# Performance work log

Measured on AMD Instinct MI355X. Metric: run time of the kernel, lower is better.

Reference implementation:

```python
import jax, jax.numpy as jnp
import numpy as np

D_IN = 768
D_SAE = 24576
BATCH = 2048
K = 64


def setup_inputs() -> dict:
    key = jax.random.key(0)
    k1, k2 = jax.random.split(key)
    x = jax.random.normal(k1, (BATCH, D_IN), dtype=jnp.float32)
    # kaiming-uniform-ish init then unit-norm rows (set_decoder_norm_to_unit_norm)
    bound = np.sqrt(6.0 / D_SAE)
    W_dec = jax.random.uniform(k2, (D_SAE, D_IN), minval=-bound, maxval=bound, dtype=jnp.float32)
    W_dec = W_dec / jnp.linalg.norm(W_dec, axis=1, keepdims=True)
    W_enc = W_dec.T  # tied at init (W_dec.t().clone())
    b_enc = jnp.zeros((D_SAE,), dtype=jnp.float32)
    b_dec = jnp.zeros((D_IN,), dtype=jnp.float32)
    return {"x": x, "W_enc": W_enc, "W_dec": W_dec, "b_enc": b_enc, "b_dec": b_dec, "k": K}


def topk_activation(pre, k):
    # torch.topk -> relu(values) -> scatter into zeros
    vals, idx = jax.lax.top_k(pre, k)            # [B, k]
    vals = jax.nn.relu(vals)
    rows = jnp.arange(pre.shape[0])[:, None]     # [B, 1]
    return jnp.zeros_like(pre).at[rows, idx].set(vals)


def reference(x, W_enc, W_dec, b_enc, b_dec, k):
    # normalize=False -> preprocess is identity
    xc = x - b_dec
    latents_pre_act = xc @ W_enc + b_enc         # [B, d_sae]
    latents = topk_activation(latents_pre_act, k)
    recons = latents @ W_dec + b_dec             # [B, d_in]
    mse_loss = jnp.sum((recons - x) ** 2)        # F.mse_loss(reduction='sum')
    return mse_loss
```

## Files before the change

### kernel.cpp

```cpp
#include <hip/hip_runtime.h>
#include <hip/hip_bf16.h>
#include <stdint.h>
#include <string.h>

#define D_IN 768
#define D_SAE 24576
#define BATCH 2048
#define TOPK 64

typedef _Float16 f16x8 __attribute__((ext_vector_type(8)));
typedef _Float16 f16x4 __attribute__((ext_vector_type(4)));
typedef float floatx4 __attribute__((ext_vector_type(4)));

#define AS1 __attribute__((address_space(1)))
#define AS3 __attribute__((address_space(3)))

__device__ __forceinline__ void load_lds16(const void* g, void* l) {
    __builtin_amdgcn_global_load_lds((AS1 void*)(g), (AS3 void*)(l), 16, 0, 0);
}

__global__ __launch_bounds__(256) void prep_x_kernel(const float* __restrict__ x,
                                                     const float* __restrict__ b_dec,
                                                     _Float16* __restrict__ xch,
                                                     float* __restrict__ out) {
    if (blockIdx.x == 0 && threadIdx.x == 0) out[0] = 0.0f;
    int i = (blockIdx.x * 256 + threadIdx.x) * 4;
    if (i >= BATCH * D_IN) return;
    int c = i % D_IN;
    float4 xv = *(const float4*)(x + i);
    float4 bv = *(const float4*)(b_dec + c);
    f16x4 h;
    h[0] = (_Float16)(xv.x - bv.x);
    h[1] = (_Float16)(xv.y - bv.y);
    h[2] = (_Float16)(xv.z - bv.z);
    h[3] = (_Float16)(xv.w - bv.w);
    *(f16x4*)(xch + i) = h;
}

__global__ __launch_bounds__(256) void transpose_kernel(const float* __restrict__ W,
                                                        _Float16* __restrict__ WT) {
    __shared__ _Float16 tile[32][33];
    int n0 = blockIdx.x * 32;
    int k0 = blockIdx.y * 32;
    int tx = threadIdx.x & 31, ty = threadIdx.x >> 5;
#pragma unroll
    for (int r = 0; r < 4; ++r) {
        int k = k0 + ty + r * 8;
        tile[ty + r * 8][tx] = (_Float16)W[(size_t)k * D_SAE + n0 + tx];
    }
    __syncthreads();
#pragma unroll
    for (int r = 0; r < 4; ++r) {
        int n = n0 + ty + r * 8;
        WT[(size_t)n * D_IN + k0 + tx] = tile[tx][ty + r * 8];
    }
}

__global__ __launch_bounds__(256) void gemm_kernel(const _Float16* __restrict__ A,
                                                   const _Float16* __restrict__ BT,
                                                   const float* __restrict__ b_enc,
                                                   unsigned short* __restrict__ pre) {
    __shared__ _Float16 As[128 * 32];
    __shared__ _Float16 Bs[128 * 32];
    const int tid = threadIdx.x;
    const int lane = tid & 63;
    const int wave = tid >> 6;
    const int m0 = blockIdx.x * 128;
    const int n0 = blockIdx.y * 128;
    const int wm = wave >> 1, wn = wave & 1;
    const int colv = lane & 15, quad = lane >> 4;

    floatx4 acc[4][4];
#pragma unroll
    for (int mi = 0; mi < 4; ++mi)
#pragma unroll
        for (int ni = 0; ni < 4; ++ni)
#pragma unroll
            for (int r = 0; r < 4; ++r) acc[mi][ni][r] = 0.0f;

    for (int kt = 0; kt < 24; ++kt) {
        const int k0 = kt * 32;
#pragma unroll
        for (int i = 0; i < 2; ++i) {
            int gw = i * 256 + wave * 64;
            int g = gw + lane;
            int r = g >> 2, kq = g & 3;
            load_lds16(A + (size_t)(m0 + r) * D_IN + k0 + kq * 8, &As[gw * 8]);
            load_lds16(BT + (size_t)(n0 + r) * D_IN + k0 + kq * 8, &Bs[gw * 8]);
        }
        __syncthreads();
        f16x8 af[4], bf[4];
#pragma unroll
        for (int mi = 0; mi < 4; ++mi)
            af[mi] = *(const f16x8*)&As[(wm * 64 + mi * 16 + colv) * 32 + quad * 8];
#pragma unroll
        for (int ni = 0; ni < 4; ++ni)
            bf[ni] = *(const f16x8*)&Bs[(wn * 64 + ni * 16 + colv) * 32 + quad * 8];
#pragma unroll
        for (int mi = 0; mi < 4; ++mi)
#pragma unroll
            for (int ni = 0; ni < 4; ++ni)
                acc[mi][ni] = __builtin_amdgcn_mfma_f32_16x16x32_f16(af[mi], bf[ni], acc[mi][ni], 0, 0, 0);
        __syncthreads();
    }
    float be[4];
#pragma unroll
    for (int ni = 0; ni < 4; ++ni) be[ni] = b_enc[n0 + wn * 64 + ni * 16 + colv];
#pragma unroll
    for (int mi = 0; mi < 4; ++mi) {
#pragma unroll
        for (int ni = 0; ni < 4; ++ni) {
            size_t base = (size_t)(m0 + wm * 64 + mi * 16 + quad * 4) * D_SAE
                        + (size_t)(n0 + wn * 64 + ni * 16 + colv);
#pragma unroll
            for (int r = 0; r < 4; ++r) {
                _Float16 h = (_Float16)(acc[mi][ni][r] + be[ni]);
                unsigned short u;
                __builtin_memcpy(&u, &h, 2);
                unsigned short key = u ^ ((u & 0x8000) ? 0xFFFFu : 0x8000u);
                pre[base + (size_t)r * D_SAE] = key;
            }
        }
    }
}

#define TKT 384
#define KPT 64
__global__ __launch_bounds__(TKT) void topk_loss_kernel(const unsigned short* __restrict__ pre,
                                                        const float* __restrict__ x,
                                                        const float* __restrict__ W_dec,
                                                        const float* __restrict__ b_dec,
                                                        float* __restrict__ out) {
    const int row = blockIdx.x;
    const int tid = threadIdx.x;
    const int lane = tid & 63, wv = tid >> 6;

    __shared__ int hist[256];
    __shared__ int wtot[6];
    __shared__ float wred[6];
    __shared__ int sh_cnt, sh_B, sh_K, na, ne;
    __shared__ int sel_idx[TOPK];
    __shared__ float sel_val[TOPK];

    const uint4* kp = (const uint4*)(pre + (size_t)row * D_SAE) + tid * 8;
    unsigned w[32];
#pragma unroll
    for (int i = 0; i < 8; ++i) {
        uint4 v = kp[i];
        w[i * 4 + 0] = v.x; w[i * 4 + 1] = v.y; w[i * 4 + 2] = v.z; w[i * 4 + 3] = v.w;
    }
    const int colbase = tid * KPT;

    if (tid == 0) sh_cnt = 0;
    __syncthreads();
    int c = 0;
#pragma unroll
    for (int q = 0; q < 32; ++q) {
        c += ((w[q] & 0xFFFFu) >= 0xC000u);
        c += ((w[q] >> 16) >= 0xC000u);
    }
#pragma unroll
    for (int off = 32; off > 0; off >>= 1) c += __shfl_down(c, off, 64);
    if (lane == 0) atomicAdd(&sh_cnt, c);
    __syncthreads();
    const unsigned lim = (sh_cnt >= TOPK) ? 0xC000u : 0u;

    if (tid < 256) hist[tid] = 0;
    __syncthreads();
#pragma unroll
    for (int q = 0; q < 32; ++q) {
        unsigned k0 = w[q] & 0xFFFFu, k1 = w[q] >> 16;
        if (k0 >= lim) atomicAdd(&hist[k0 >> 8], 1);
        if (k1 >= lim) atomicAdd(&hist[k1 >> 8], 1);
    }
    __syncthreads();
    int K = TOPK;
    {
        int h = 0, s = 0;
        if (tid < 256) { h = hist[tid]; s = h; }
#pragma unroll
        for (int off = 1; off < 64; off <<= 1) {
            int v = __shfl_down(s, off, 64);
            if (lane + off < 64) s += v;
        }
        if (tid < 256 && lane == 0) wtot[wv] = s;
        __syncthreads();
        if (tid < 256) {
            for (int w2 = wv + 1; w2 < 4; ++w2) s += wtot[w2];
            int G = s - h;
            if (G < K && s >= K) { sh_B = tid; sh_K = K - G; }
        }
        __syncthreads();
    }
    const unsigned B = (unsigned)sh_B;
    K = sh_K;
    __syncthreads();

    if (tid < 256) hist[tid] = 0;
    __syncthreads();
#pragma unroll
    for (int q = 0; q < 32; ++q) {
        unsigned k0 = w[q] & 0xFFFFu, k1 = w[q] >> 16;
        if ((k0 >> 8) == B) atomicAdd(&hist[k0 & 0xFF], 1);
        if ((k1 >> 8) == B) atomicAdd(&hist[k1 & 0xFF], 1);
    }
    __syncthreads();
    {
        int h = 0, s = 0;
        if (tid < 256) { h = hist[tid]; s = h; }
#pragma unroll
        for (int off = 1; off < 64; off <<= 1) {
            int v = __shfl_down(s, off, 64);
            if (lane + off < 64) s += v;
        }
        if (tid < 256 && lane == 0) wtot[wv] = s;
        __syncthreads();
        if (tid < 256) {
            for (int w2 = wv + 1; w2 < 4; ++w2) s += wtot[w2];
            int G = s - h;
            if (G < K && s >= K) { sh_B = tid; sh_K = K - G; }
        }
        __syncthreads();
    }
    const unsigned T = (B << 8) | (unsigned)sh_B;
    const int K2 = sh_K;
    const int nGreater = TOPK - K2;

    if (tid == 0) { na = 0; ne = 0; }
    __syncthreads();
#pragma unroll
    for (int q = 0; q < 32; ++q) {
#pragma unroll
        for (int half = 0; half < 2; ++half) {
            unsigned k = half ? (w[q] >> 16) : (w[q] & 0xFFFFu);
            int col = colbase + q * 2 + half;
            int slot = -1;
            if (k > T) slot = atomicAdd(&na, 1);
            else if (k == T) {
                int e = atomicAdd(&ne, 1);
                if (e < K2) slot = nGreater + e;
            }
            if (slot >= 0) {
                unsigned short u = (unsigned short)((k & 0x8000u) ? (k ^ 0x8000u) : (k ^ 0xFFFFu));
                _Float16 h;
                __builtin_memcpy(&h, &u, 2);
                float v = (float)h;
                sel_idx[slot] = col;
                sel_val[slot] = fmaxf(v, 0.0f);
            }
        }
    }
    __syncthreads();

    const int c0 = tid, c1 = tid + TKT;
    const float* xr = x + (size_t)row * D_IN;
    float r0 = b_dec[c0], r1 = b_dec[c1];
#pragma unroll 8
    for (int s = 0; s < TOPK; ++s) {
        float v = sel_val[s];
        const float* wr = W_dec + (size_t)sel_idx[s] * D_IN;
        r0 += v * wr[c0];
        r1 += v * wr[c1];
    }
    float d0 = r0 - xr[c0], d1 = r1 - xr[c1];
    float local = d0 * d0 + d1 * d1;

#pragma unroll
    for (int off = 32; off > 0; off >>= 1) local += __shfl_down(local, off, 64);
    if (lane == 0) wred[wv] = local;
    __syncthreads();
    if (tid == 0) {
        float s = 0.0f;
#pragma unroll
        for (int i = 0; i < 6; ++i) s += wred[i];
        atomicAdd(out, s);
    }
}

extern "C" void kernel_launch(void* const* d_in, const int* in_sizes, int n_in,
                              void* d_out, int out_size, void* d_ws, size_t ws_size,
                              hipStream_t stream) {
    const float* x     = (const float*)d_in[0];
    const float* W_enc = (const float*)d_in[1];
    const float* W_dec = (const float*)d_in[2];
    const float* b_enc = (const float*)d_in[3];
    const float* b_dec = (const float*)d_in[4];
    float* out = (float*)d_out;

    char* ws = (char*)d_ws;
    _Float16* xch      = (_Float16*)ws;
    _Float16* WT       = (_Float16*)(ws + 3145728);
    unsigned short* pre = (unsigned short*)(ws + 3145728 + 37748736);

    prep_x_kernel<<<1536, 256, 0, stream>>>(x, b_dec, xch, out);
    transpose_kernel<<<dim3(D_SAE / 32, D_IN / 32), 256, 0, stream>>>(W_enc, WT);
    gemm_kernel<<<dim3(BATCH / 128, D_SAE / 128), 256, 0, stream>>>(xch, WT, b_enc, pre);
    topk_loss_kernel<<<BATCH, TKT, 0, stream>>>(pre, x, W_dec, b_dec, out);
}
```

Measured before the change: 362.2 us.

## Collect top-k candidates above threshold in GEMM epilogue, select from compact list

The GEMM epilogue now appends every pre-activation whose key is at least fp16 2.0 to a per-row candidate list (key plus column), using a global atomic counter per row. The top-k kernel then runs its radix select over the small candidate list in LDS instead of rescanning the full 24576-wide row. It falls back to the full row if the count is below k or above capacity. This trades many global atomics in the GEMM epilogue for a large cut in top-k read traffic and work. The block size also drops to 256 threads.

```diff
diff --git a/kernel.cpp b/kernel.cpp
--- a/kernel.cpp
+++ b/kernel.cpp
@@ -7,6 +7,8 @@
 #define D_SAE 24576
 #define BATCH 2048
 #define TOPK 64
+#define CAP 1024
+#define KEY_LIM 0xC000u
 
 typedef _Float16 f16x8 __attribute__((ext_vector_type(8)));
 typedef _Float16 f16x4 __attribute__((ext_vector_type(4)));
@@ -22,9 +24,12 @@
 __global__ __launch_bounds__(256) void prep_x_kernel(const float* __restrict__ x,
                                                      const float* __restrict__ b_dec,
                                                      _Float16* __restrict__ xch,
+                                                     int* __restrict__ cnt,
                                                      float* __restrict__ out) {
-    if (blockIdx.x == 0 && threadIdx.x == 0) out[0] = 0.0f;
-    int i = (blockIdx.x * 256 + threadIdx.x) * 4;
+    int t = blockIdx.x * 256 + threadIdx.x;
+    if (t == 0) out[0] = 0.0f;
+    if (t < BATCH) cnt[t] = 0;
+    int i = t * 4;
     if (i >= BATCH * D_IN) return;
     int c = i % D_IN;
     float4 xv = *(const float4*)(x + i);
@@ -59,7 +64,9 @@
 __global__ __launch_bounds__(256) void gemm_kernel(const _Float16* __restrict__ A,
                                                    const _Float16* __restrict__ BT,
                                                    const float* __restrict__ b_enc,
-                                                   unsigned short* __restrict__ pre) {
+                                                   unsigned short* __restrict__ pre,
+                                                   int* __restrict__ cnt,
+                                                   unsigned* __restrict__ cand) {
     __shared__ _Float16 As[128 * 32];
     __shared__ _Float16 Bs[128 * 32];
     const int tid = threadIdx.x;
@@ -110,23 +117,29 @@
     for (int mi = 0; mi < 4; ++mi) {
 #pragma unroll
         for (int ni = 0; ni < 4; ++ni) {
-            size_t base = (size_t)(m0 + wm * 64 + mi * 16 + quad * 4) * D_SAE
-                        + (size_t)(n0 + wn * 64 + ni * 16 + colv);
+            const int n_g = n0 + wn * 64 + ni * 16 + colv;
+            const int r_g0 = m0 + wm * 64 + mi * 16 + quad * 4;
+            size_t base = (size_t)r_g0 * D_SAE + (size_t)n_g;
 #pragma unroll
             for (int r = 0; r < 4; ++r) {
                 _Float16 h = (_Float16)(acc[mi][ni][r] + be[ni]);
                 unsigned short u;
                 __builtin_memcpy(&u, &h, 2);
-                unsigned short key = u ^ ((u & 0x8000) ? 0xFFFFu : 0x8000u);
-                pre[base + (size_t)r * D_SAE] = key;
+                unsigned key = (unsigned)(u ^ ((u & 0x8000) ? 0xFFFFu : 0x8000u));
+                pre[base + (size_t)r * D_SAE] = (unsigned short)key;
+                if (key >= KEY_LIM) {
+                    int row = r_g0 + r;
+                    int slot = atomicAdd(&cnt[row], 1);
+                    if (slot < CAP) cand[(size_t)row * CAP + slot] = (key << 16) | (unsigned)n_g;
+                }
             }
         }
     }
 }
 
-#define TKT 384
-#define KPT 64
-__global__ __launch_bounds__(TKT) void topk_loss_kernel(const unsigned short* __restrict__ pre,
+__global__ __launch_bounds__(256) void topk_loss_kernel(const unsigned short* __restrict__ pre,
+                                                        const unsigned* __restrict__ cand,
+                                                        const int* __restrict__ cnt,
                                                         const float* __restrict__ x,
                                                         const float* __restrict__ W_dec,
                                                         const float* __restrict__ b_dec,
@@ -135,146 +148,120 @@
     const int tid = threadIdx.x;
     const int lane = tid & 63, wv = tid >> 6;
 
+    __shared__ unsigned cl[CAP];
     __shared__ int hist[256];
-    __shared__ int wtot[6];
-    __shared__ float wred[6];
-    __shared__ int sh_cnt, sh_B, sh_K, na, ne;
+    __shared__ int wtot[4];
+    __shared__ float wred[4];
+    __shared__ int sh_B, sh_K, na, ne;
     __shared__ int sel_idx[TOPK];
     __shared__ float sel_val[TOPK];
 
-    const uint4* kp = (const uint4*)(pre + (size_t)row * D_SAE) + tid * 8;
-    unsigned w[32];
-#pragma unroll
-    for (int i = 0; i < 8; ++i) {
-        uint4 v = kp[i];
-        w[i * 4 + 0] = v.x; w[i * 4 + 1] = v.y; w[i * 4 + 2] = v.z; w[i * 4 + 3] = v.w;
-    }
-    const int colbase = tid * KPT;
-
-    if (tid == 0) sh_cnt = 0;
-    __syncthreads();
-    int c = 0;
-#pragma unroll
-    for (int q = 0; q < 32; ++q) {
-        c += ((w[q] & 0xFFFFu) >= 0xC000u);
-        c += ((w[q] >> 16) >= 0xC000u);
-    }
-#pragma unroll
-    for (int off = 32; off > 0; off >>= 1) c += __shfl_down(c, off, 64);
-    if (lane == 0) atomicAdd(&sh_cnt, c);
-    __syncthreads();
-    const unsigned lim = (sh_cnt >= TOPK) ? 0xC000u : 0u;
-
-    if (tid < 256) hist[tid] = 0;
-    __syncthreads();
-#pragma unroll
-    for (int q = 0; q < 32; ++q) {
-        unsigned k0 = w[q] & 0xFFFFu, k1 = w[q] >> 16;
-        if (k0 >= lim) atomicAdd(&hist[k0 >> 8], 1);
-        if (k1 >= lim) atomicAdd(&hist[k1 >> 8], 1);
-    }
-    __syncthreads();
+    const int n_raw = cnt[row];
+    const bool fast = (n_raw >= TOPK && n_raw <= CAP);
+    const int N = fast ? n_raw : D_SAE;
+    const unsigned short* prow = pre + (size_t)row * D_SAE;
+
+    if (fast) {
+        const unsigned* cr = cand + (size_t)row * CAP;
+        for (int i = tid; i < N; i += 256) cl[i] = cr[i];
+    }
+    __syncthreads();
+
     int K = TOPK;
+    unsigned B = 0, T = 0;
+    int K2 = 0;
+
+    hist[tid] = 0;
+    __syncthreads();
+    for (int i = tid; i < N; i += 256) {
+        unsigned k = fast ? (cl[i] >> 24) : ((unsigned)prow[i] >> 8);
+        atomicAdd(&hist[k], 1);
+    }
+    __syncthreads();
     {
-        int h = 0, s = 0;
-        if (tid < 256) { h = hist[tid]; s = h; }
+        int h = hist[tid], s = h;
 #pragma unroll
         for (int off = 1; off < 64; off <<= 1) {
             int v = __shfl_down(s, off, 64);
             if (lane + off < 64) s += v;
         }
-        if (tid < 256 && lane == 0) wtot[wv] = s;
-        __syncthreads();
-        if (tid < 256) {
-            for (int w2 = wv + 1; w2 < 4; ++w2) s += wtot[w2];
-            int G = s - h;
-            if (G < K && s >= K) { sh_B = tid; sh_K = K - G; }
-        }
-        __syncthreads();
-    }
-    const unsigned B = (unsigned)sh_B;
+        if (lane == 0) wtot[wv] = s;
+        __syncthreads();
+        for (int w2 = wv + 1; w2 < 4; ++w2) s += wtot[w2];
+        int G = s - h;
+        if (G < K && s >= K) { sh_B = tid; sh_K = K - G; }
+        __syncthreads();
+    }
+    B = (unsigned)sh_B;
     K = sh_K;
     __syncthreads();
 
-    if (tid < 256) hist[tid] = 0;
-    __syncthreads();
-#pragma unroll
-    for (int q = 0; q < 32; ++q) {
-        unsigned k0 = w[q] & 0xFFFFu, k1 = w[q] >> 16;
-        if ((k0 >> 8) == B) atomicAdd(&hist[k0 & 0xFF], 1);
-        if ((k1 >> 8) == B) atomicAdd(&hist[k1 & 0xFF], 1);
+    hist[tid] = 0;
+    __syncthreads();
+    for (int i = tid; i < N; i += 256) {
+        unsigned k = fast ? (cl[i] >> 16) : (unsigned)prow[i];
+        if ((k >> 8) == B) atomicAdd(&hist[k & 0xFF], 1);
     }
     __syncthreads();
     {
-        int h = 0, s = 0;
-        if (tid < 256) { h = hist[tid]; s = h; }
+        int h = hist[tid], s = h;
 #pragma unroll
         for (int off = 1; off < 64; off <<= 1) {
             int v = __shfl_down(s, off, 64);
             if (lane + off < 64) s += v;
         }
-        if (tid < 256 && lane == 0) wtot[wv] = s;
-        __syncthreads();
-        if (tid < 256) {
-            for (int w2 = wv + 1; w2 < 4; ++w2) s += wtot[w2];
-            int G = s - h;
-            if (G < K && s >= K) { sh_B = tid; sh_K = K - G; }
-        }
-        __syncthreads();
-    }
-    const unsigned T = (B << 8) | (unsigned)sh_B;
-    const int K2 = sh_K;
+        if (lane == 0) wtot[wv] = s;
+        __syncthreads();
+        for (int w2 = wv + 1; w2 < 4; ++w2) s += wtot[w2];
+        int G = s - h;
+        if (G < K && s >= K) { sh_B = tid; sh_K = K - G; }
+        __syncthreads();
+    }
+    T = (B << 8) | (unsigned)sh_B;
+    K2 = sh_K;
     const int nGreater = TOPK - K2;
 
     if (tid == 0) { na = 0; ne = 0; }
     __syncthreads();
-#pragma unroll
-    for (int q = 0; q < 32; ++q) {
-#pragma unroll
-        for (int half = 0; half < 2; ++half) {
-            unsigned k = half ? (w[q] >> 16) : (w[q] & 0xFFFFu);
-            int col = colbase + q * 2 + half;
-            int slot = -1;
-            if (k > T) slot = atomicAdd(&na, 1);
-            else if (k == T) {
-                int e = atomicAdd(&ne, 1);
-                if (e < K2) slot = nGreater + e;
-            }
-            if (slot >= 0) {
-                unsigned short u = (unsigned short)((k & 0x8000u) ? (k ^ 0x8000u) : (k ^ 0xFFFFu));
-                _Float16 h;
-                __builtin_memcpy(&h, &u, 2);
-                float v = (float)h;
-                sel_idx[slot] = col;
-                sel_val[slot] = fmaxf(v, 0.0f);
-            }
-        }
-    }
-    __syncthreads();
-
-    const int c0 = tid, c1 = tid + TKT;
+    for (int i = tid; i < N; i += 256) {
+        unsigned k; int col;
+        if (fast) { unsigned v = cl[i]; k = v >> 16; col = (int)(v & 0xFFFFu); }
+        else      { k = (unsigned)prow[i]; col = i; }
+        int slot = -1;
+        if (k > T) slot = atomicAdd(&na, 1);
+        else if (k == T) {
+            int e = atomicAdd(&ne, 1);
+            if (e < K2) slot = nGreater + e;
+        }
+        if (slot >= 0) {
+            unsigned short u = (unsigned short)((k & 0x8000u) ? (k ^ 0x8000u) : (k ^ 0xFFFFu));
+            _Float16 h;
+            __builtin_memcpy(&h, &u, 2);
+            sel_idx[slot] = col;
+            sel_val[slot] = fmaxf((float)h, 0.0f);
+        }
+    }
+    __syncthreads();
+
+    const int c0 = tid, c1 = tid + 256, c2 = tid + 512;
     const float* xr = x + (size_t)row * D_IN;
-    float r0 = b_dec[c0], r1 = b_dec[c1];
+    float r0 = b_dec[c0], r1 = b_dec[c1], r2 = b_dec[c2];
 #pragma unroll 8
     for (int s = 0; s < TOPK; ++s) {
         float v = sel_val[s];
         const float* wr = W_dec + (size_t)sel_idx[s] * D_IN;
         r0 += v * wr[c0];
         r1 += v * wr[c1];
-    }
-    float d0 = r0 - xr[c0], d1 = r1 - xr[c1];
-    float local = d0 * d0 + d1 * d1;
+        r2 += v * wr[c2];
+    }
+    float d0 = r0 - xr[c0], d1 = r1 - xr[c1], d2 = r2 - xr[c2];
+    float local = d0 * d0 + d1 * d1 + d2 * d2;
 
 #pragma unroll
     for (int off = 32; off > 0; off >>= 1) local += __shfl_down(local, off, 64);
     if (lane == 0) wred[wv] = local;
     __syncthreads();
-    if (tid == 0) {
-        float s = 0.0f;
-#pragma unroll
-        for (int i = 0; i < 6; ++i) s += wred[i];
-        atomicAdd(out, s);
-    }
+    if (tid == 0) atomicAdd(out, wred[0] + wred[1] + wred[2] + wred[3]);
 }
 
 extern "C" void kernel_launch(void* const* d_in, const int* in_sizes, int n_in,
@@ -288,12 +275,14 @@
     float* out = (float*)d_out;
 
     char* ws = (char*)d_ws;
-    _Float16* xch      = (_Float16*)ws;
-    _Float16* WT       = (_Float16*)(ws + 3145728);
+    _Float16* xch       = (_Float16*)ws;
+    _Float16* WT        = (_Float16*)(ws + 3145728);
     unsigned short* pre = (unsigned short*)(ws + 3145728 + 37748736);
-
-    prep_x_kernel<<<1536, 256, 0, stream>>>(x, b_dec, xch, out);
+    int* cnt            = (int*)(ws + 3145728 + 37748736 + 100663296);
+    unsigned* cand      = (unsigned*)(ws + 3145728 + 37748736 + 100663296 + 8192);
+
+    prep_x_kernel<<<1536, 256, 0, stream>>>(x, b_dec, xch, cnt, out);
     transpose_kernel<<<dim3(D_SAE / 32, D_IN / 32), 256, 0, stream>>>(W_enc, WT);
-    gemm_kernel<<<dim3(BATCH / 128, D_SAE / 128), 256, 0, stream>>>(xch, WT, b_enc, pre);
-    topk_loss_kernel<<<BATCH, TKT, 0, stream>>>(pre, x, W_dec, b_dec, out);
-}
+    gemm_kernel<<<dim3(BATCH / 128, D_SAE / 128), 256, 0, stream>>>(xch, WT, b_enc, pre, cnt, cand);
+    topk_loss_kernel<<<BATCH, 256, 0, stream>>>(pre, cand, cnt, x, W_dec, b_dec, out);
+}
```

Result: slower. 693.5 us (+91.5%).
